# Optimization experiments

Hardware: AMD Instinct MI355X
Metric: run time of the kernel (lower is better)

## Reference

```python
import jax, jax.numpy as jnp
import numpy as np

# config matching init_kwargs
B = 16
NEI = 30
S1 = 2 * NEI + 1          # 61: image side, also local attn window size
KS = 3
SZ = 2 * KS + 1           # 7: conv kernel size
PCH = SZ * SZ             # 49 conv out channels
D = 128                   # d_model
H = 8                     # heads (all local, since n_local_attn_heads == heads)
DH = D // H               # 16
L = 4                     # depth
S = S1 * S1               # 3721 sequence length
NW = S // S1              # 61 windows of size 61
WIN = S1
POS = 4096
FF = 4 * D
EPS = 1e-5


def _sincos(n, d):
    pos = np.arange(n)[:, None].astype(np.float64)
    i = np.arange(d)[None, :]
    ang = pos / np.power(10000.0, 2 * (i // 2) / d)
    tab = np.zeros((n, d))
    tab[:, 0::2] = np.sin(ang[:, 0::2])
    tab[:, 1::2] = np.cos(ang[:, 1::2])
    return jnp.asarray(tab, jnp.float32)


def _ln(x, s, b):
    m = x.mean(-1, keepdims=True)
    v = ((x - m) ** 2).mean(-1, keepdims=True)
    return (x - m) / jnp.sqrt(v + EPS) * s + b


def _local_mask():
    # valid-key mask per window over [prev | self | next] blocks; edges padded
    ones = jnp.ones((NW, WIN), jnp.float32)
    p = jnp.pad(ones, ((1, 1), (0, 0)))
    return jnp.concatenate([p[:-2], p[1:-1], p[2:]], axis=1) > 0.5


def _local_attn(x, wq, wk, wv, wo, wob):
    # non-causal windowed attention, look_backward=1, look_forward=1 (lucidrains LocalAttention)
    bq = x.shape[0]

    def to_windows(w):
        y = (x @ w).reshape(bq, S, H, DH).transpose(0, 2, 1, 3)
        return y.reshape(bq * H, NW, WIN, DH)

    q = to_windows(wq) * (DH ** -0.5)
    k = to_windows(wk)
    v = to_windows(wv)

    def gather(t):
        p = jnp.pad(t, ((0, 0), (1, 1), (0, 0), (0, 0)))
        return jnp.concatenate([p[:, :-2], p[:, 1:-1], p[:, 2:]], axis=2)

    bk, bv = gather(k), gather(v)
    scores = jnp.einsum('bnqd,bnkd->bnqk', q, bk)
    scores = jnp.where(_local_mask()[None, :, None, :], scores, -1e9)
    attn = jax.nn.softmax(scores, axis=-1)
    o = jnp.einsum('bnqk,bnkd->bnqd', attn, bv)
    o = o.reshape(bq, H, S, DH).transpose(0, 2, 1, 3).reshape(bq, S, D)
    return o @ wo + wob


def _forward(x, conv_w, conv_b, lt_w, lt_b, pos_table, ln1_s, ln1_b, wq, wk, wv, wo, wo_b,
             ln2_s, ln2_b, ff_w1, ff_b1, ff_w2, ff_b2, pre_w1, pre_b1, pre_w2, pre_b2):
    # conv patch extraction, 'same' padding, ReLU
    p = jax.lax.conv_general_dilated(x[:, None], conv_w, (1, 1), [(KS, KS), (KS, KS)],
                                     dimension_numbers=('NCHW', 'OIHW', 'NCHW'))
    p = jax.nn.relu(p + conv_b[None, :, None, None])
    p = p.reshape(B, PCH, S).transpose(0, 2, 1)       # [B, S, 49]
    h = p @ lt_w + lt_b + pos_table[:S][None]         # [B, S, D]
    for i in range(L):
        h = h + _local_attn(_ln(h, ln1_s[i], ln1_b[i]), wq[i], wk[i], wv[i], wo[i], wo_b[i])
        hn = _ln(h, ln2_s[i], ln2_b[i])
        h = h + (jax.nn.gelu(hn @ ff_w1[i] + ff_b1[i], approximate=False) @ ff_w2[i] + ff_b2[i])
    out = jax.nn.relu(h @ pre_w1 + pre_b1) @ pre_w2 + pre_b2  # [B, S, 1]
    return out.reshape(B, S1, S1)


def setup_inputs() -> dict:
    key = jax.random.key(0)
    ks = jax.random.split(key, 12)
    g = lambda k, sh, sc=0.02: jax.random.normal(k, sh, jnp.float32) * sc
    return {
        'x': jax.random.normal(ks[0], (B, S1, S1), jnp.float32),
        'conv_w': g(ks[1], (PCH, 1, SZ, SZ), 0.1),
        'conv_b': jnp.zeros((PCH,), jnp.float32),
        'lt_w': g(ks[2], (PCH, D)),
        'lt_b': jnp.zeros((D,), jnp.float32),
        'pos_table': _sincos(POS, D),
        'ln1_s': jnp.ones((L, D), jnp.float32), 'ln1_b': jnp.zeros((L, D), jnp.float32),
        'wq': g(ks[3], (L, D, D)), 'wk': g(ks[4], (L, D, D)), 'wv': g(ks[5], (L, D, D)),
        'wo': g(ks[6], (L, D, D)), 'wo_b': jnp.zeros((L, D), jnp.float32),
        'ln2_s': jnp.ones((L, D), jnp.float32), 'ln2_b': jnp.zeros((L, D), jnp.float32),
        'ff_w1': g(ks[7], (L, D, FF)), 'ff_b1': jnp.zeros((L, FF), jnp.float32),
        'ff_w2': g(ks[8], (L, FF, D)), 'ff_b2': jnp.zeros((L, D), jnp.float32),
        'pre_w1': g(ks[9], (D, D)), 'pre_b1': jnp.zeros((D,), jnp.float32),
        'pre_w2': g(ks[10], (D, 1)), 'pre_b2': jnp.zeros((1,), jnp.float32),
    }


def reference(x, conv_w, conv_b, lt_w, lt_b, pos_table, ln1_s, ln1_b, wq, wk, wv, wo, wo_b,
              ln2_s, ln2_b, ff_w1, ff_b1, ff_w2, ff_b2, pre_w1, pre_b1, pre_w2, pre_b2):
    return _forward(x, conv_w, conv_b, lt_w, lt_b, pos_table, ln1_s, ln1_b, wq, wk, wv, wo, wo_b,
                    ln2_s, ln2_b, ff_w1, ff_b1, ff_w2, ff_b2, pre_w1, pre_b1, pre_w2, pre_b2)
```

## Files before the change

kernel.cpp:

```cpp
#include <hip/hip_runtime.h>
#include <hip/hip_bf16.h>
#include <math.h>
#include <string.h>

#define B_   16
#define S1_  61
#define S_   3721
#define D_   128
#define H_   8
#define NW_  61
#define FF_  512
#define BS_  (B_*S_)

#define SC_LOG2E 0.36067376022224085f

typedef unsigned int   uint32;
typedef unsigned short ushort16;
typedef __attribute__((ext_vector_type(8))) short  short8;
typedef __attribute__((ext_vector_type(4))) float  floatx4;
typedef __attribute__((ext_vector_type(4))) uint32 uint32x4;

__device__ __forceinline__ ushort16 f2bf(float f) {
  uint32 u = __float_as_uint(f);
  uint32 r = u + 0x7fffu + ((u >> 16) & 1u);
  return (ushort16)(r >> 16);
}
__device__ __forceinline__ uint32 pkbf(float a, float b) {
  __hip_bfloat162 t = __float22bfloat162_rn(float2{a, b});
  uint32 r;
  memcpy(&r, &t, 4);
  return r;
}
__device__ __forceinline__ short8 mk8(uint32 a, uint32 b) {
  uint32x4 v = {a, b, 0u, 0u};
  return __builtin_bit_cast(short8, v);
}
__device__ __forceinline__ void gl2lds16(const void* g, void* l) {
  __builtin_amdgcn_global_load_lds(
      (const __attribute__((address_space(1))) unsigned int*)g,
      (__attribute__((address_space(3))) unsigned int*)l, 16, 0, 0);
}

__global__ __launch_bounds__(256) void prep_w(
    const float* __restrict__ wq, const float* __restrict__ wk, const float* __restrict__ wv,
    const float* __restrict__ wo, const float* __restrict__ w1, const float* __restrict__ w2,
    const float* __restrict__ lt, const float* __restrict__ pw1,
    const float* __restrict__ cw, const float* __restrict__ cb,
    ushort16* __restrict__ qkv_t, ushort16* __restrict__ wo_t, ushort16* __restrict__ w1_t,
    ushort16* __restrict__ w2_t, ushort16* __restrict__ lt_t, ushort16* __restrict__ pw1_t,
    ushort16* __restrict__ wc_t, float* __restrict__ cb_pad) {
  int i = blockIdx.x * 256 + threadIdx.x;
  if (i < 196608) {
    int l = i / 49152, r = i % 49152;
    int n = r / 128, k = r % 128;
    const float* src = (n < 128) ? wq : (n < 256) ? wk : wv;
    qkv_t[i] = f2bf(src[(l * 128 + k) * 128 + (n & 127)]);
  } else if (i < 262144) {
    int j = i - 196608;
    int l = j / 16384, r = j % 16384;
    int n = r / 128, k = r % 128;
    wo_t[j] = f2bf(wo[(l * 128 + k) * 128 + n]);
  } else if (i < 524288) {
    int j = i - 262144;
    int l = j / 65536, r = j % 65536;
    int n = r / 128, k = r % 128;
    w1_t[j] = f2bf(w1[(size_t)l * 65536 + k * 512 + n]);
  } else if (i < 786432) {
    int j = i - 524288;
    int l = j / 65536, r = j % 65536;
    int n = r / 512, k = r % 512;
    w2_t[j] = f2bf(w2[(size_t)l * 65536 + k * 128 + n]);
  } else if (i < 794624) {
    int j = i - 786432;
    int n = j / 64, k = j % 64;
    lt_t[j] = f2bf(k < 49 ? lt[k * 128 + n] : 0.f);
  } else if (i < 811008) {
    int j = i - 794624;
    int n = j / 128, k = j % 128;
    pw1_t[j] = f2bf(pw1[k * 128 + n]);
  } else if (i < 815104) {
    int j = i - 811008;
    int n = j >> 6, k = j & 63;
    wc_t[j] = f2bf((n < 49 && k < 49) ? cw[n * 49 + k] : 0.f);
  } else if (i < 815168) {
    int j = i - 815104;
    cb_pad[j] = (j < 49) ? cb[j] : 0.f;
  }
}

__global__ __launch_bounds__(256) void im2col_k(const float* __restrict__ x,
                                                ushort16* __restrict__ X) {
  int t = blockIdx.x * 256 + threadIdx.x;
  if (t >= BS_ * 64) return;
  int tap = t & 63;
  int row = t >> 6;
  if (tap >= 49) { X[t] = 0; return; }
  int b = row / S_, s = row % S_;
  int i = s / S1_, j = s % S1_;
  int di = tap / 7, dj = tap % 7;
  int ii = i + di - 3, jj = j + dj - 3;
  float v = 0.f;
  if ((unsigned)ii < (unsigned)S1_ && (unsigned)jj < (unsigned)S1_)
    v = x[(b * S1_ + ii) * S1_ + jj];
  X[t] = f2bf(v);
}

enum { E_BF16 = 0, E_H0LN = 1, E_RESLN = 2, E_GELU = 3, E_RELU = 4, E_RESBF = 5, E_QKV = 6 };

template <int EPI, int K>
__global__ __launch_bounds__(512) void gemm_bf16(
    const ushort16* __restrict__ A, int lda,
    const ushort16* __restrict__ Bt, int ldbt,
    float* __restrict__ H,
    ushort16* __restrict__ Cb, int ldc,
    const float* __restrict__ bias,
    const float* __restrict__ pos,
    const float* __restrict__ ls,
    const float* __restrict__ lb,
    int M, int N) {
  __shared__ ushort16 As[8192];
  __shared__ ushort16 Bs[8192];
  __shared__ float stats[128][2][2];
  int bm = blockIdx.y * 128, bn = blockIdx.x * 128;
  int tid = threadIdx.x;
  int lane = tid & 63, wave = tid >> 6;
  int wm = (wave >> 1) * 32, wn = (wave & 1) * 64;
  int ln = lane & 15, qd = lane >> 4;
  int lr = lane >> 3;
  int cg = (lane & 7) ^ lr;

  const ushort16* aP[2];
  const ushort16* bP[2];
  #pragma unroll
  for (int u = 0; u < 2; u++) {
    int s = wave * 2 + u;
    int ar = bm + s * 8 + lr; if (ar > M - 1) ar = M - 1;
    int br = bn + s * 8 + lr; if (br > N - 1) br = N - 1;
    aP[u] = A  + (size_t)ar * lda  + cg * 8;
    bP[u] = Bt + (size_t)br * ldbt + cg * 8;
  }

  floatx4 acc[2][4] = {};
  #pragma unroll
  for (int kc = 0; kc < K; kc += 64) {
    #pragma unroll
    for (int u = 0; u < 2; u++) {
      int s = wave * 2 + u;
      gl2lds16(aP[u] + kc, &As[s * 512]);
      gl2lds16(bP[u] + kc, &Bs[s * 512]);
    }
    __syncthreads();
    #pragma unroll
    for (int ks = 0; ks < 64; ks += 32) {
      int cb0 = ks >> 3;
      short8 af[2], bf[4];
      #pragma unroll
      for (int i = 0; i < 2; i++) {
        int row = wm + i * 16 + ln;
        af[i] = *(const short8*)&As[row * 64 + (((cb0 + qd) ^ (ln & 7)) * 8)];
      }
      #pragma unroll
      for (int j = 0; j < 4; j++) {
        int row = wn + j * 16 + ln;
        bf[j] = *(const short8*)&Bs[row * 64 + (((cb0 + qd) ^ (ln & 7)) * 8)];
      }
      #pragma unroll
      for (int i = 0; i < 2; i++)
        #pragma unroll
        for (int j = 0; j < 4; j++)
          acc[i][j] = __builtin_amdgcn_mfma_f32_16x16x32_bf16(af[i], bf[j], acc[i][j], 0, 0, 0);
    }
    if (kc + 64 < K) __syncthreads();
  }

  if (EPI == E_H0LN || EPI == E_RESLN) {
    float lsv[4], lbv[4];
    #pragma unroll
    for (int j = 0; j < 4; j++) {
      int gn = wn + j * 16 + ln;
      lsv[j] = ls[gn]; lbv[j] = lb[gn];
    }
    int wI = wn >> 6;
    #pragma unroll
    for (int i = 0; i < 2; i++) {
      #pragma unroll
      for (int r = 0; r < 4; r++) {
        int lrow = wm + i * 16 + qd * 4 + r;
        int gm = bm + lrow;
        int gmc = (gm < M) ? gm : (M - 1);
        float s1 = 0.f, s2 = 0.f;
        #pragma unroll
        for (int j = 0; j < 4; j++) {
          int gn = wn + j * 16 + ln;
          float v = acc[i][j][r];
          float g;
          if (EPI == E_H0LN) g = v + bias[gn] + pos[(size_t)(gmc % S_) * 128 + gn];
          else               g = H[(size_t)gmc * 128 + gn] + v + bias[gn];
          acc[i][j][r] = g;
          if (gm < M) H[(size_t)gm * 128 + gn] = g;
          s1 += g; s2 = fmaf(g, g, s2);
        }
        #pragma unroll
        for (int off = 1; off <= 8; off <<= 1) {
          s1 += __shfl_xor(s1, off);
          s2 += __shfl_xor(s2, off);
        }
        if (ln == 0) { stats[lrow][wI][0] = s1; stats[lrow][wI][1] = s2; }
      }
    }
    __syncthreads();
    #pragma unroll
    for (int i = 0; i < 2; i++) {
      #pragma unroll
      for (int r = 0; r < 4; r++) {
        int lrow = wm + i * 16 + qd * 4 + r;
        int gm = bm + lrow;
        if (gm >= M) continue;
        float s1 = stats[lrow][0][0] + stats[lrow][1][0];
        float s2 = stats[lrow][0][1] + stats[lrow][1][1];
        float mean = s1 * (1.f / 128.f);
        float var  = s2 * (1.f / 128.f) - mean * mean;
        float inv  = rsqrtf(fmaxf(var, 0.f) + 1e-5f);
        #pragma unroll
        for (int j = 0; j < 4; j++) {
          int gn = wn + j * 16 + ln;
          Cb[(size_t)gm * 128 + gn] = f2bf((acc[i][j][r] - mean) * inv * lsv[j] + lbv[j]);
        }
      }
    }
  } else {
    float qsc = (EPI == E_QKV && bn == 0) ? SC_LOG2E : 1.0f;
    #pragma unroll
    for (int i = 0; i < 2; i++) {
      #pragma unroll
      for (int r = 0; r < 4; r++) {
        int gm = bm + wm + i * 16 + qd * 4 + r;
        if (gm >= M) continue;
        #pragma unroll
        for (int j = 0; j < 4; j++) {
          int gn = bn + wn + j * 16 + ln;
          if (gn >= N) continue;
          float v = acc[i][j][r];
          if (EPI == E_BF16) {
            Cb[(size_t)gm * ldc + gn] = f2bf(v);
          } else if (EPI == E_QKV) {
            Cb[(size_t)gm * ldc + gn] = f2bf(v * qsc);
          } else if (EPI == E_GELU) {
            float g = v + bias[gn];
            g = 0.5f * g * (1.f + erff(g * 0.70710678118654752f));
            Cb[(size_t)gm * ldc + gn] = f2bf(g);
          } else if (EPI == E_RELU) {
            float g = fmaxf(v + bias[gn], 0.f);
            Cb[(size_t)gm * ldc + gn] = f2bf(g);
          } else if (EPI == E_RESBF) {
            size_t o = (size_t)gm * 128 + gn;
            float g = H[o] + v + bias[gn];
            H[o] = g;
            Cb[(size_t)gm * ldc + gn] = f2bf(g);
          }
        }
      }
    }
  }
}

__global__ __launch_bounds__(64) void attn3(const ushort16* __restrict__ qkv,
                                            ushort16* __restrict__ o) {
  int bid = blockIdx.x;
  int xcd = bid & 7, idx = bid >> 3;
  int w  = idx % NW_;
  int bh = xcd * 16 + idx / NW_;
  int hh = bh & 7, b = bh >> 3;
  __shared__ ushort16 Kl[192][16];
  __shared__ ushort16 Vl[192][16];
  int lane = threadIdx.x;
  int qcol = lane & 15, quad = lane >> 4;

  #pragma unroll
  for (int c = 0; c < 6; c++) {
    int e = c * 64 + lane;
    int j = e >> 1, half = (e & 1) * 8;
    int krow = (w - 1) * 61 + j;
    if (krow < 0) krow = 0;
    if (krow > S_ - 1) krow = S_ - 1;
    const ushort16* gk = qkv + ((size_t)(b * S_ + krow) * 384 + 128 + hh * 16 + half);
    gl2lds16(gk,       &Kl[0][0] + c * 512);
    gl2lds16(gk + 128, &Vl[0][0] + c * 512);
  }

  short8 qf[4];
  #pragma unroll
  for (int qt = 0; qt < 4; qt++) {
    int qloc = qt * 16 + qcol;
    if (qloc > 60) qloc = 60;
    const uint32* qp = (const uint32*)(qkv + ((size_t)(b * S_ + w * 61 + qloc) * 384 + hh * 16 + quad * 4));
    qf[qt] = mk8(qp[0], qp[1]);
  }
  __syncthreads();

  int j0 = (w == 0) ? 61 : 0;
  int j1 = (w == NW_ - 1) ? 122 : 183;
  int kt0 = (w == 0) ? 3 : 0;
  int kt1 = (w == NW_ - 1) ? 8 : 12;

  floatx4 oacc[4];
  #pragma unroll
  for (int qt = 0; qt < 4; qt++) { oacc[qt][0]=0.f; oacc[qt][1]=0.f; oacc[qt][2]=0.f; oacc[qt][3]=0.f; }
  float lsum[4] = {0.f, 0.f, 0.f, 0.f};
  const floatx4 zero4 = {0.f, 0.f, 0.f, 0.f};

  for (int kt = kt0; kt < kt1; kt++) {
    const uint32* kp = (const uint32*)&Kl[kt * 16 + qcol][quad * 4];
    short8 kf = mk8(kp[0], kp[1]);

    int kb = kt * 16 + quad * 4;
    uint32 va = (uint32)Vl[kb + 0][qcol] | ((uint32)Vl[kb + 1][qcol] << 16);
    uint32 vb = (uint32)Vl[kb + 2][qcol] | ((uint32)Vl[kb + 3][qcol] << 16);
    short8 vf = mk8(va, vb);

    floatx4 sacc[4];
    #pragma unroll
    for (int qt = 0; qt < 4; qt++)
      sacc[qt] = __builtin_amdgcn_mfma_f32_16x16x32_bf16(kf, qf[qt], zero4, 0, 0, 0);

    uint32 m01 = (((unsigned)(kb + 0 - j0) < (unsigned)(j1 - j0)) ? 0x0000ffffu : 0u)
               | (((unsigned)(kb + 1 - j0) < (unsigned)(j1 - j0)) ? 0xffff0000u : 0u);
    uint32 m23 = (((unsigned)(kb + 2 - j0) < (unsigned)(j1 - j0)) ? 0x0000ffffu : 0u)
               | (((unsigned)(kb + 3 - j0) < (unsigned)(j1 - j0)) ? 0xffff0000u : 0u);
    #pragma unroll
    for (int qt = 0; qt < 4; qt++) {
      float e0 = __builtin_amdgcn_exp2f(sacc[qt][0]);
      float e1 = __builtin_amdgcn_exp2f(sacc[qt][1]);
      float e2 = __builtin_amdgcn_exp2f(sacc[qt][2]);
      float e3 = __builtin_amdgcn_exp2f(sacc[qt][3]);
      uint32 p01 = pkbf(e0, e1) & m01;
      uint32 p23 = pkbf(e2, e3) & m23;
      lsum[qt] += (__uint_as_float(p01 << 16) + __uint_as_float(p01 & 0xffff0000u))
                + (__uint_as_float(p23 << 16) + __uint_as_float(p23 & 0xffff0000u));
      oacc[qt] = __builtin_amdgcn_mfma_f32_16x16x32_bf16(mk8(p01, p23), vf, oacc[qt], 0, 0, 0);
    }
  }

  #pragma unroll
  for (int qt = 0; qt < 4; qt++) {
    float l = lsum[qt];
    l += __shfl_xor(l, 16);
    l += __shfl_xor(l, 32);
    lsum[qt] = 1.0f / fmaxf(l, 1e-30f);
  }
  #pragma unroll
  for (int qt = 0; qt < 4; qt++) {
    #pragma unroll
    for (int r = 0; r < 4; r++) {
      int qloc = qt * 16 + quad * 4 + r;
      float invl = __shfl(lsum[qt], quad * 4 + r);
      if (qloc < 61) {
        size_t row = (size_t)b * S_ + w * 61 + qloc;
        o[row * 128 + hh * 16 + qcol] = f2bf(oacc[qt][r] * invl);
      }
    }
  }
}

__global__ __launch_bounds__(256) void head2(const ushort16* __restrict__ t2,
                                             const float* __restrict__ w2,
                                             const float* __restrict__ b2,
                                             float* __restrict__ out, int rows) {
  int wv = (blockIdx.x * 256 + threadIdx.x) >> 6;
  int lane = threadIdx.x & 63;
  if (wv >= rows) return;
  uint32 u = *(const uint32*)(t2 + (size_t)wv * 128 + lane * 2);
  float a = __uint_as_float(u << 16) * w2[lane * 2]
          + __uint_as_float(u & 0xffff0000u) * w2[lane * 2 + 1];
  #pragma unroll
  for (int off = 32; off; off >>= 1) a += __shfl_xor(a, off);
  if (lane == 0) out[wv] = a + b2[0];
}

extern "C" void kernel_launch(void* const* d_in, const int* in_sizes, int n_in,
                              void* d_out, int out_size, void* d_ws, size_t ws_size,
                              hipStream_t stream) {
  const float* x      = (const float*)d_in[0];
  const float* conv_w = (const float*)d_in[1];
  const float* conv_b = (const float*)d_in[2];
  const float* lt_w   = (const float*)d_in[3];
  const float* lt_b   = (const float*)d_in[4];
  const float* pos    = (const float*)d_in[5];
  const float* ln1_s  = (const float*)d_in[6];
  const float* ln1_b  = (const float*)d_in[7];
  const float* wq     = (const float*)d_in[8];
  const float* wk     = (const float*)d_in[9];
  const float* wv     = (const float*)d_in[10];
  const float* wo     = (const float*)d_in[11];
  const float* wo_b   = (const float*)d_in[12];
  const float* ln2_s  = (const float*)d_in[13];
  const float* ln2_b  = (const float*)d_in[14];
  const float* ff_w1  = (const float*)d_in[15];
  const float* ff_b1  = (const float*)d_in[16];
  const float* ff_w2  = (const float*)d_in[17];
  const float* ff_b2  = (const float*)d_in[18];
  const float* pre_w1 = (const float*)d_in[19];
  const float* pre_b1 = (const float*)d_in[20];
  const float* pre_w2 = (const float*)d_in[21];
  const float* pre_b2 = (const float*)d_in[22];

  char* ws = (char*)d_ws;
  const size_t SZ_H   = (size_t)BS_ * 128 * 4;
  const size_t SZ_HN  = (size_t)BS_ * 128 * 2;
  const size_t SZ_QKV = (size_t)BS_ * 384 * 2;
  const size_t SZ_O   = (size_t)BS_ * 128 * 2;
  float*    h    = (float*)ws;
  ushort16* hn   = (ushort16*)(ws + SZ_H);
  ushort16* qkvb = (ushort16*)(ws + SZ_H + SZ_HN);
  ushort16* ob   = (ushort16*)(ws + SZ_H + SZ_HN + SZ_QKV);
  char*     wsw  = ws + SZ_H + SZ_HN + SZ_QKV + SZ_O;
  ushort16* qkv_t = (ushort16*)(wsw);
  ushort16* wo_t  = qkv_t + 196608;
  ushort16* w1_t  = wo_t  + 65536;
  ushort16* w2_t  = w1_t  + 262144;
  ushort16* lt_t  = w2_t  + 262144;
  ushort16* pw1_t = lt_t  + 8192;
  ushort16* wc_t  = pw1_t + 16384;
  float*    cb_pad = (float*)(wc_t + 4096);
  ushort16* X  = ob;
  ushort16* p  = qkvb;
  ushort16* t  = qkvb;
  ushort16* hb = hn;
  ushort16* t2 = ob;

  prep_w<<<dim3(3185), 256, 0, stream>>>(wq, wk, wv, wo, ff_w1, ff_w2, lt_w, pre_w1,
                                         conv_w, conv_b,
                                         qkv_t, wo_t, w1_t, w2_t, lt_t, pw1_t, wc_t, cb_pad);
  im2col_k<<<dim3((BS_ * 64 + 255) / 256), 256, 0, stream>>>(x, X);

  const int MB = (BS_ + 127) / 128;
  int lnBlocks = (BS_ + 3) / 4;
  gemm_bf16<E_RELU, 64><<<dim3(1, MB), 512, 0, stream>>>(X, 64, wc_t, 64, nullptr, p, 64,
                                                         cb_pad, nullptr, nullptr, nullptr, BS_, 64);
  gemm_bf16<E_H0LN, 64><<<dim3(1, MB), 512, 0, stream>>>(p, 64, lt_t, 64, h, hn, 128,
                                                         lt_b, pos, ln1_s, ln1_b, BS_, 128);

  for (int l = 0; l < 4; l++) {
    gemm_bf16<E_QKV, 128><<<dim3(3, MB), 512, 0, stream>>>(hn, 128, qkv_t + (size_t)l * 49152, 128,
                                                           nullptr, qkvb, 384, nullptr, nullptr,
                                                           nullptr, nullptr, BS_, 384);
    attn3<<<dim3(B_ * H_ * NW_), 64, 0, stream>>>(qkvb, ob);
    gemm_bf16<E_RESLN, 128><<<dim3(1, MB), 512, 0, stream>>>(ob, 128, wo_t + (size_t)l * 16384, 128,
                                                             h, hn, 128, wo_b + l * 128, nullptr,
                                                             ln2_s + l * 128, ln2_b + l * 128, BS_, 128);
    gemm_bf16<E_GELU, 128><<<dim3(4, MB), 512, 0, stream>>>(hn, 128, w1_t + (size_t)l * 65536, 128,
                                                            nullptr, t, 512, ff_b1 + l * 512, nullptr,
                                                            nullptr, nullptr, BS_, 512);
    if (l < 3) {
      gemm_bf16<E_RESLN, 512><<<dim3(1, MB), 512, 0, stream>>>(t, 512, w2_t + (size_t)l * 65536, 512,
                                                               h, hn, 128, ff_b2 + l * 128, nullptr,
                                                               ln1_s + (l + 1) * 128, ln1_b + (l + 1) * 128,
                                                               BS_, 128);
    } else {
      gemm_bf16<E_RESBF, 512><<<dim3(1, MB), 512, 0, stream>>>(t, 512, w2_t + (size_t)l * 65536, 512,
                                                               h, hb, 128, ff_b2 + l * 128, nullptr,
                                                               nullptr, nullptr, BS_, 128);
    }
  }
  gemm_bf16<E_RELU, 128><<<dim3(1, MB), 512, 0, stream>>>(hb, 128, pw1_t, 128,
                                                          nullptr, t2, 128, pre_b1, nullptr,
                                                          nullptr, nullptr, BS_, 128);
  head2<<<dim3(lnBlocks), 256, 0, stream>>>(t2, pre_w2, pre_b2, (float*)d_out, BS_);
}
```

Baseline: 732.1 us.

## Store residual stream in bf16 and fuse prediction head into GEMM epilogue

The fp32 residual stream h becomes a bf16 buffer, which halves its read/write traffic in every residual+LayerNorm epilogue. The final pre_w2 projection is folded into the pre_w1 GEMM epilogue: each row's ReLU output is dotted with pre_w2 through shuffle reductions and written directly to the output, so the separate head kernel and its intermediate buffer are gone. The cost is precision, since the residual now accumulates in bf16 across layers and rounding error may build up.

```diff
diff --git a/kernel.cpp b/kernel.cpp
--- a/kernel.cpp
+++ b/kernel.cpp
@@ -24,6 +24,9 @@
   uint32 u = __float_as_uint(f);
   uint32 r = u + 0x7fffu + ((u >> 16) & 1u);
   return (ushort16)(r >> 16);
+}
+__device__ __forceinline__ float bf2f(ushort16 s) {
+  return __uint_as_float(((uint32)s) << 16);
 }
 __device__ __forceinline__ uint32 pkbf(float a, float b) {
   __hip_bfloat162 t = __float22bfloat162_rn(float2{a, b});
@@ -105,18 +108,20 @@
   X[t] = f2bf(v);
 }
 
-enum { E_BF16 = 0, E_H0LN = 1, E_RESLN = 2, E_GELU = 3, E_RELU = 4, E_RESBF = 5, E_QKV = 6 };
+enum { E_BF16 = 0, E_H0LN = 1, E_RESLN = 2, E_GELU = 3, E_RELU = 4, E_RESBF = 5,
+       E_QKV = 6, E_HEAD = 7 };
 
 template <int EPI, int K>
 __global__ __launch_bounds__(512) void gemm_bf16(
     const ushort16* __restrict__ A, int lda,
     const ushort16* __restrict__ Bt, int ldbt,
-    float* __restrict__ H,
+    ushort16* __restrict__ Hb,
     ushort16* __restrict__ Cb, int ldc,
     const float* __restrict__ bias,
     const float* __restrict__ pos,
     const float* __restrict__ ls,
     const float* __restrict__ lb,
+    float* __restrict__ Fout,
     int M, int N) {
   __shared__ ushort16 As[8192];
   __shared__ ushort16 Bs[8192];
@@ -173,12 +178,14 @@
     if (kc + 64 < K) __syncthreads();
   }
 
-  if (EPI == E_H0LN || EPI == E_RESLN) {
+  if (EPI == E_H0LN || EPI == E_RESLN || EPI == E_RESBF) {
     float lsv[4], lbv[4];
-    #pragma unroll
-    for (int j = 0; j < 4; j++) {
-      int gn = wn + j * 16 + ln;
-      lsv[j] = ls[gn]; lbv[j] = lb[gn];
+    if (EPI != E_RESBF) {
+      #pragma unroll
+      for (int j = 0; j < 4; j++) {
+        int gn = wn + j * 16 + ln;
+        lsv[j] = ls[gn]; lbv[j] = lb[gn];
+      }
     }
     int wI = wn >> 6;
     #pragma unroll
@@ -195,17 +202,65 @@
           float v = acc[i][j][r];
           float g;
           if (EPI == E_H0LN) g = v + bias[gn] + pos[(size_t)(gmc % S_) * 128 + gn];
-          else               g = H[(size_t)gmc * 128 + gn] + v + bias[gn];
+          else               g = bf2f(Hb[(size_t)gmc * 128 + gn]) + v + bias[gn];
           acc[i][j][r] = g;
-          if (gm < M) H[(size_t)gm * 128 + gn] = g;
+          if (gm < M) Hb[(size_t)gm * 128 + gn] = f2bf(g);
           s1 += g; s2 = fmaf(g, g, s2);
         }
-        #pragma unroll
-        for (int off = 1; off <= 8; off <<= 1) {
-          s1 += __shfl_xor(s1, off);
-          s2 += __shfl_xor(s2, off);
+        if (EPI != E_RESBF) {
+          #pragma unroll
+          for (int off = 1; off <= 8; off <<= 1) {
+            s1 += __shfl_xor(s1, off);
+            s2 += __shfl_xor(s2, off);
+          }
+          if (ln == 0) { stats[lrow][wI][0] = s1; stats[lrow][wI][1] = s2; }
         }
-        if (ln == 0) { stats[lrow][wI][0] = s1; stats[lrow][wI][1] = s2; }
+      }
+    }
+    if (EPI != E_RESBF) {
+      __syncthreads();
+      #pragma unroll
+      for (int i = 0; i < 2; i++) {
+        #pragma unroll
+        for (int r = 0; r < 4; r++) {
+          int lrow = wm + i * 16 + qd * 4 + r;
+          int gm = bm + lrow;
+          if (gm >= M) continue;
+          float s1 = stats[lrow][0][0] + stats[lrow][1][0];
+          float s2 = stats[lrow][0][1] + stats[lrow][1][1];
+          float mean = s1 * (1.f / 128.f);
+          float var  = s2 * (1.f / 128.f) - mean * mean;
+          float inv  = rsqrtf(fmaxf(var, 0.f) + 1e-5f);
+          #pragma unroll
+          for (int j = 0; j < 4; j++) {
+            int gn = wn + j * 16 + ln;
+            Cb[(size_t)gm * 128 + gn] = f2bf((acc[i][j][r] - mean) * inv * lsv[j] + lbv[j]);
+          }
+        }
+      }
+    }
+  } else if (EPI == E_HEAD) {
+    float w2v[4];
+    #pragma unroll
+    for (int j = 0; j < 4; j++) {
+      int gn = wn + j * 16 + ln;
+      w2v[j] = ls[gn];
+    }
+    int wI = wn >> 6;
+    #pragma unroll
+    for (int i = 0; i < 2; i++) {
+      #pragma unroll
+      for (int r = 0; r < 4; r++) {
+        int lrow = wm + i * 16 + qd * 4 + r;
+        float s1 = 0.f;
+        #pragma unroll
+        for (int j = 0; j < 4; j++) {
+          int gn = wn + j * 16 + ln;
+          s1 = fmaf(fmaxf(acc[i][j][r] + bias[gn], 0.f), w2v[j], s1);
+        }
+        #pragma unroll
+        for (int off = 1; off <= 8; off <<= 1) s1 += __shfl_xor(s1, off);
+        if (ln == 0) stats[lrow][wI][0] = s1;
       }
     }
     __syncthreads();
@@ -215,17 +270,8 @@
       for (int r = 0; r < 4; r++) {
         int lrow = wm + i * 16 + qd * 4 + r;
         int gm = bm + lrow;
-        if (gm >= M) continue;
-        float s1 = stats[lrow][0][0] + stats[lrow][1][0];
-        float s2 = stats[lrow][0][1] + stats[lrow][1][1];
-        float mean = s1 * (1.f / 128.f);
-        float var  = s2 * (1.f / 128.f) - mean * mean;
-        float inv  = rsqrtf(fmaxf(var, 0.f) + 1e-5f);
-        #pragma unroll
-        for (int j = 0; j < 4; j++) {
-          int gn = wn + j * 16 + ln;
-          Cb[(size_t)gm * 128 + gn] = f2bf((acc[i][j][r] - mean) * inv * lsv[j] + lbv[j]);
-        }
+        if (gm < M && ln == 0 && wI == 0)
+          Fout[gm] = stats[lrow][0][0] + stats[lrow][1][0] + lb[0];
       }
     }
   } else {
@@ -252,11 +298,6 @@
           } else if (EPI == E_RELU) {
             float g = fmaxf(v + bias[gn], 0.f);
             Cb[(size_t)gm * ldc + gn] = f2bf(g);
-          } else if (EPI == E_RESBF) {
-            size_t o = (size_t)gm * 128 + gn;
-            float g = H[o] + v + bias[gn];
-            H[o] = g;
-            Cb[(size_t)gm * ldc + gn] = f2bf(g);
           }
         }
       }
@@ -360,21 +401,6 @@
       }
     }
   }
-}
-
-__global__ __launch_bounds__(256) void head2(const ushort16* __restrict__ t2,
-                                             const float* __restrict__ w2,
-                                             const float* __restrict__ b2,
-                                             float* __restrict__ out, int rows) {
-  int wv = (blockIdx.x * 256 + threadIdx.x) >> 6;
-  int lane = threadIdx.x & 63;
-  if (wv >= rows) return;
-  uint32 u = *(const uint32*)(t2 + (size_t)wv * 128 + lane * 2);
-  float a = __uint_as_float(u << 16) * w2[lane * 2]
-          + __uint_as_float(u & 0xffff0000u) * w2[lane * 2 + 1];
-  #pragma unroll
-  for (int off = 32; off; off >>= 1) a += __shfl_xor(a, off);
-  if (lane == 0) out[wv] = a + b2[0];
 }
 
 extern "C" void kernel_launch(void* const* d_in, const int* in_sizes, int n_in,
@@ -405,15 +431,14 @@
   const float* pre_b2 = (const float*)d_in[22];
 
   char* ws = (char*)d_ws;
-  const size_t SZ_H   = (size_t)BS_ * 128 * 4;
-  const size_t SZ_HN  = (size_t)BS_ * 128 * 2;
+  const size_t SZ_HB  = (size_t)BS_ * 128 * 2;
   const size_t SZ_QKV = (size_t)BS_ * 384 * 2;
   const size_t SZ_O   = (size_t)BS_ * 128 * 2;
-  float*    h    = (float*)ws;
-  ushort16* hn   = (ushort16*)(ws + SZ_H);
-  ushort16* qkvb = (ushort16*)(ws + SZ_H + SZ_HN);
-  ushort16* ob   = (ushort16*)(ws + SZ_H + SZ_HN + SZ_QKV);
-  char*     wsw  = ws + SZ_H + SZ_HN + SZ_QKV + SZ_O;
+  ushort16* h    = (ushort16*)ws;
+  ushort16* hn   = (ushort16*)(ws + SZ_HB);
+  ushort16* qkvb = (ushort16*)(ws + 2 * SZ_HB);
+  ushort16* ob   = (ushort16*)(ws + 2 * SZ_HB + SZ_QKV);
+  char*     wsw  = ws + 2 * SZ_HB + SZ_QKV + SZ_O;
   ushort16* qkv_t = (ushort16*)(wsw);
   ushort16* wo_t  = qkv_t + 196608;
   ushort16* w1_t  = wo_t  + 65536;
@@ -425,8 +450,6 @@
   ushort16* X  = ob;
   ushort16* p  = qkvb;
   ushort16* t  = qkvb;
-  ushort16* hb = hn;
-  ushort16* t2 = ob;
 
   prep_w<<<dim3(3185), 256, 0, stream>>>(wq, wk, wv, wo, ff_w1, ff_w2, lt_w, pre_w1,
                                          conv_w, conv_b,
@@ -434,36 +457,36 @@
   im2col_k<<<dim3((BS_ * 64 + 255) / 256), 256, 0, stream>>>(x, X);
 
   const int MB = (BS_ + 127) / 128;
-  int lnBlocks = (BS_ + 3) / 4;
   gemm_bf16<E_RELU, 64><<<dim3(1, MB), 512, 0, stream>>>(X, 64, wc_t, 64, nullptr, p, 64,
-                                                         cb_pad, nullptr, nullptr, nullptr, BS_, 64);
+                                                         cb_pad, nullptr, nullptr, nullptr, nullptr,
+                                                         BS_, 64);
   gemm_bf16<E_H0LN, 64><<<dim3(1, MB), 512, 0, stream>>>(p, 64, lt_t, 64, h, hn, 128,
-                                                         lt_b, pos, ln1_s, ln1_b, BS_, 128);
+                                                         lt_b, pos, ln1_s, ln1_b, nullptr, BS_, 128);
 
   for (int l = 0; l < 4; l++) {
     gemm_bf16<E_QKV, 128><<<dim3(3, MB), 512, 0, stream>>>(hn, 128, qkv_t + (size_t)l * 49152, 128,
                                                            nullptr, qkvb, 384, nullptr, nullptr,
-                                                           nullptr, nullptr, BS_, 384);
+                                                           nullptr, nullptr, nullptr, BS_, 384);
     attn3<<<dim3(B_ * H_ * NW_), 64, 0, stream>>>(qkvb, ob);
     gemm_bf16<E_RESLN, 128><<<dim3(1, MB), 512, 0, stream>>>(ob, 128, wo_t + (size_t)l * 16384, 128,
                                                              h, hn, 128, wo_b + l * 128, nullptr,
-                                                             ln2_s + l * 128, ln2_b + l * 128, BS_, 128);
+                                                             ln2_s + l * 128, ln2_b + l * 128, nullptr,
+                                                             BS_, 128);
     gemm_bf16<E_GELU, 128><<<dim3(4, MB), 512, 0, stream>>>(hn, 128, w1_t + (size_t)l * 65536, 128,
                                                             nullptr, t, 512, ff_b1 + l * 512, nullptr,
-                                                            nullptr, nullptr, BS_, 512);
+                                                            nullptr, nullptr, nullptr, BS_, 512);
     if (l < 3) {
       gemm_bf16<E_RESLN, 512><<<dim3(1, MB), 512, 0, stream>>>(t, 512, w2_t + (size_t)l * 65536, 512,
                                                                h, hn, 128, ff_b2 + l * 128, nullptr,
                                                                ln1_s + (l + 1) * 128, ln1_b + (l + 1) * 128,
-                                                               BS_, 128);
+                                                               nullptr, BS_, 128);
     } else {
       gemm_bf16<E_RESBF, 512><<<dim3(1, MB), 512, 0, stream>>>(t, 512, w2_t + (size_t)l * 65536, 512,
-                                                               h, hb, 128, ff_b2 + l * 128, nullptr,
-                                                               nullptr, nullptr, BS_, 128);
-    }
-  }
-  gemm_bf16<E_RELU, 128><<<dim3(1, MB), 512, 0, stream>>>(hb, 128, pw1_t, 128,
-                                                          nullptr, t2, 128, pre_b1, nullptr,
-                                                          nullptr, nullptr, BS_, 128);
-  head2<<<dim3(lnBlocks), 256, 0, stream>>>(t2, pre_w2, pre_b2, (float*)d_out, BS_);
-}
+                                                               h, nullptr, 128, ff_b2 + l * 128, nullptr,
+                                                               nullptr, nullptr, nullptr, BS_, 128);
+    }
+  }
+  gemm_bf16<E_HEAD, 128><<<dim3(1, MB), 512, 0, stream>>>(h, 128, pw1_t, 128,
+                                                          nullptr, nullptr, 128, pre_b1, nullptr,
+                                                          pre_w2, pre_b2, (float*)d_out, BS_, 128);
+}
```

Measured after the change: 679.8 us. 1.08x faster.
